# Kernel optimization log

Hardware: AMD Instinct MI355X
Metric: run time of the kernel (lower is better)

The kernel has to match this reference:

```python
import jax, jax.numpy as jnp
import numpy as np

N_NODES = 100000
D = 512
N_EDGES = 150000
N_PRED = 200000
EPS = 1e-12  # F.normalize default eps


def setup_inputs() -> dict:
    key = jax.random.key(0)
    ks = jax.random.split(key, 8)
    scale = 1.0 / np.sqrt(D)
    return {
        "x": jax.random.normal(ks[0], (N_NODES, D), dtype=jnp.float32),
        "edge_index": jax.random.randint(ks[1], (2, N_EDGES), 0, N_NODES, dtype=jnp.int64),
        "edge_weight": jax.random.uniform(ks[2], (N_EDGES,), dtype=jnp.float32),
        "pred_edges": jax.random.randint(ks[3], (2, N_PRED), 0, N_NODES, dtype=jnp.int64),
        "W1": jax.random.normal(ks[4], (D, D), dtype=jnp.float32) * scale,
        "b1": jnp.zeros((D,), jnp.float32),
        "W2": jax.random.normal(ks[5], (D, D), dtype=jnp.float32) * scale,
        "b2": jnp.zeros((D,), jnp.float32),
        "Wf": jax.random.normal(ks[6], (D, 2), dtype=jnp.float32) * scale,
        "bf": jnp.zeros((2,), jnp.float32),
    }


def gcn_conv(x, W, b, row, col, w, n):
    """PyG GCNConv with normalize=True: add self-loops (weight 1),
    symmetric deg^-1/2 normalization, message = norm * (xW)[row], scatter-add to col."""
    loop = jnp.arange(n)
    row2 = jnp.concatenate([row, loop])
    col2 = jnp.concatenate([col, loop])
    w2 = jnp.concatenate([w, jnp.ones((n,), x.dtype)])
    deg = jax.ops.segment_sum(w2, col2, num_segments=n)
    dinv = jnp.where(deg > 0, jax.lax.rsqrt(jnp.maximum(deg, EPS)), 0.0)
    norm = dinv[row2] * w2 * dinv[col2]  # [E+n]
    h = x @ W  # [n, out]
    out = jax.ops.segment_sum(norm[:, None] * h[row2], col2, num_segments=n)
    return out + b


def res_block(x, W, b, row, col, w, n):
    h = jax.nn.relu(gcn_conv(x, W, b, row, col, w, n))
    # dropout is identity in eval mode; then row-wise L2 normalize (F.normalize)
    nrm = jnp.maximum(jnp.linalg.norm(h, axis=1, keepdims=True), EPS)
    h = h / nrm
    return (h + x) * 0.5  # residual average (use_identity=True)


def reference(x, edge_index, edge_weight, pred_edges, W1, b1, W2, b2, Wf, bf):
    n = x.shape[0]
    row, col = edge_index[0], edge_index[1]
    h = res_block(x, W1, b1, row, col, edge_weight, n)
    h = res_block(h, W2, b2, row, col, edge_weight, n)
    h = gcn_conv(h, Wf, bf, row, col, edge_weight, n)
    h = jax.nn.log_softmax(h, axis=1)  # [n, 2]
    # DotProductPredictor, vectorized: h[u]*h[v]*(-1) per predictor edge
    return -(h[pred_edges[0]] * h[pred_edges[1]])  # [N_PRED, 2]
```

## Files before the change

kernel.cpp:

```cpp
#include <hip/hip_runtime.h>
#include <hip/hip_bf16.h>
#include <math.h>

typedef __bf16 bf16x8 __attribute__((ext_vector_type(8)));
typedef float f32x4 __attribute__((ext_vector_type(4)));
struct __align__(16) US8 { unsigned short v[8]; };

typedef __attribute__((address_space(1))) const unsigned short GUS;
typedef __attribute__((address_space(3))) unsigned short LUS;
static __device__ __forceinline__ void gload16(const unsigned short* g, unsigned short* l) {
    __builtin_amdgcn_global_load_lds((GUS*)g, (LUS*)l, 16, 0, 0);
}

static __device__ __forceinline__ unsigned short f2bf(float f) {
    unsigned int u = __float_as_uint(f);
    unsigned int r = (u + 0x7fffu + ((u >> 16) & 1u)) >> 16;
    return (unsigned short)r;
}
static __device__ __forceinline__ float bf2f(unsigned short u) {
    return __uint_as_float(((unsigned int)u) << 16);
}

__global__ void cvt_bf16_kernel(const float* __restrict__ in, unsigned short* __restrict__ outb,
                                int total8) {
    int i = blockIdx.x * 256 + threadIdx.x;
    if (i < total8) {
        const float4* p = (const float4*)(in + (size_t)i * 8);
        float4 a = p[0], b = p[1];
        US8 o;
        o.v[0] = f2bf(a.x); o.v[1] = f2bf(a.y); o.v[2] = f2bf(a.z); o.v[3] = f2bf(a.w);
        o.v[4] = f2bf(b.x); o.v[5] = f2bf(b.y); o.v[6] = f2bf(b.z); o.v[7] = f2bf(b.w);
        *(US8*)(outb + (size_t)i * 8) = o;
    }
}

__global__ void init_kernel(float* deg, int* cnt, int* cursor, int M) {
    int i = blockIdx.x * 256 + threadIdx.x;
    if (i < M) { deg[i] = 1.0f; cnt[i] = 0; cursor[i] = 0; }
}
__global__ void deg_cnt_kernel(const int* __restrict__ ei, const float* __restrict__ ew,
                               float* deg, int* cnt, int E) {
    int e = blockIdx.x * 256 + threadIdx.x;
    if (e < E) {
        int c = ei[E + e];
        atomicAdd(&deg[c], ew[e]);
        atomicAdd(&cnt[c], 1);
    }
}
__global__ void dinv_kernel(const float* __restrict__ deg, float* dinv, int M) {
    int i = blockIdx.x * 256 + threadIdx.x;
    if (i < M) dinv[i] = rsqrtf(deg[i]);
}

__global__ void chunk_sum_kernel(const int* __restrict__ cnt, int* partial, int M) {
    __shared__ int sd[256];
    int t = threadIdx.x;
    int i = blockIdx.x * 256 + t;
    sd[t] = (i < M) ? cnt[i] : 0;
    __syncthreads();
    for (int s = 128; s > 0; s >>= 1) {
        if (t < s) sd[t] += sd[t + s];
        __syncthreads();
    }
    if (t == 0) partial[blockIdx.x] = sd[0];
}
__global__ void scan_partial_kernel(int* partial, int NB) {
    __shared__ int sd[512];
    int t = threadIdx.x;
    int v = (t < NB) ? partial[t] : 0;
    sd[t] = v;
    __syncthreads();
    for (int o = 1; o < 512; o <<= 1) {
        int add = (t >= o) ? sd[t - o] : 0;
        __syncthreads();
        sd[t] += add;
        __syncthreads();
    }
    if (t < NB) partial[t] = sd[t] - v;
}
__global__ void rowptr_kernel(const int* __restrict__ cnt, const int* __restrict__ partial,
                              int* rowptr, int M, int E) {
    __shared__ int sd[256];
    int t = threadIdx.x;
    int i = blockIdx.x * 256 + t;
    int v = (i < M) ? cnt[i] : 0;
    sd[t] = v;
    __syncthreads();
    for (int o = 1; o < 256; o <<= 1) {
        int add = (t >= o) ? sd[t - o] : 0;
        __syncthreads();
        sd[t] += add;
        __syncthreads();
    }
    if (i < M) rowptr[i] = partial[blockIdx.x] + sd[t] - v;
    if (i == M - 1) rowptr[M] = E;
}
__global__ void csr_fill_kernel(const int* __restrict__ ei, const float* __restrict__ ew,
                                const float* __restrict__ dinv, const int* __restrict__ rowptr,
                                int* cursor, int* src, float* cf, int E) {
    int e = blockIdx.x * 256 + threadIdx.x;
    if (e < E) {
        int r = ei[e], c = ei[E + e];
        int k = atomicAdd(&cursor[c], 1);
        int pos = rowptr[c] + k;
        src[pos] = r;
        cf[pos] = dinv[r] * ew[e] * dinv[c];
    }
}

__global__ void agg_gather_kernel(const unsigned short* __restrict__ xin, const int* __restrict__ rowptr,
                                  const int* __restrict__ src, const float* __restrict__ cf,
                                  const float* __restrict__ dinv,
                                  unsigned short* __restrict__ abf, int M) {
    int row = blockIdx.x * 4 + (threadIdx.x >> 6);
    if (row >= M) return;
    int lane = threadIdx.x & 63;
    US8 v = *(const US8*)(xin + ((size_t)row << 9) + lane * 8);
    float d = dinv[row];
    float s = d * d;
    float a[8];
    #pragma unroll
    for (int t = 0; t < 8; t++) a[t] = s * bf2f(v.v[t]);
    int beg = rowptr[row], end = rowptr[row + 1];
    for (int j = beg; j < end; j++) {
        int r = src[j];
        float coef = cf[j];
        US8 u = *(const US8*)(xin + ((size_t)r << 9) + lane * 8);
        #pragma unroll
        for (int t = 0; t < 8; t++) a[t] += coef * bf2f(u.v[t]);
    }
    US8 o;
    #pragma unroll
    for (int t = 0; t < 8; t++) o.v[t] = f2bf(a[t]);
    *(US8*)(abf + ((size_t)row << 9) + lane * 8) = o;
}

__global__ void transpose_cvt_kernel(const float* __restrict__ W, unsigned short* __restrict__ BT) {
    int idx = blockIdx.x * 256 + threadIdx.x;
    int n = idx >> 9, k = idx & 511;
    BT[idx] = f2bf(W[k * 512 + n]);
}

__global__ __launch_bounds__(512, 4) void gemm_epi_kernel(
    const unsigned short* __restrict__ A,
    const unsigned short* __restrict__ BT,
    const float* __restrict__ bias,
    const unsigned short* __restrict__ xin,
    unsigned short* __restrict__ outp,
    int M) {
    __shared__ __align__(16) unsigned short As[2][64 * 32];
    __shared__ __align__(16) unsigned short Bs[2][512 * 32];
    __shared__ float red[8 * 64];
    __shared__ float invn[64];

    const int tid  = threadIdx.x;
    const int m0   = blockIdx.x * 64;
    const int wave = tid >> 6;
    const int lane = tid & 63;
    const int q    = lane >> 4;
    const int r    = lane & 15;

    f32x4 acc[4][4];
    #pragma unroll
    for (int mt = 0; mt < 4; mt++)
        #pragma unroll
        for (int nt = 0; nt < 4; nt++) acc[mt][nt] = (f32x4){0.f, 0.f, 0.f, 0.f};

    const int fr  = (r + (r >> 2)) & 3;
    const int kcp = q ^ fr;

    auto stage = [&](int ks, int buf) {
        const int k0 = ks * 32;
        unsigned short* Ab = &As[buf][0];
        unsigned short* Bb = &Bs[buf][0];
        #pragma unroll
        for (int j = 0; j < 4; j++) {
            int c0 = j * 512 + wave * 64;
            int c  = c0 + lane;
            if (c0 < 256) {
                int row = c >> 2, kl = c & 3;
                int kc = kl ^ ((row + (row >> 2)) & 3);
                gload16(A + (((size_t)(m0 + row)) << 9) + k0 + kc * 8, Ab + c0 * 8);
            } else {
                int cb = c - 256, cb0 = c0 - 256;
                int n = cb >> 2, kl = cb & 3;
                int kc = kl ^ ((n + (n >> 2)) & 3);
                gload16(BT + (((size_t)n) << 9) + k0 + kc * 8, Bb + cb0 * 8);
            }
        }
        if (wave < 4) {
            int cb0 = 1792 + wave * 64;
            int cb = cb0 + lane;
            int n = cb >> 2, kl = cb & 3;
            int kc = kl ^ ((n + (n >> 2)) & 3);
            gload16(BT + (((size_t)n) << 9) + k0 + kc * 8, Bb + cb0 * 8);
        }
    };

    stage(0, 0);
    for (int ks = 0; ks < 16; ks++) {
        const int cur = ks & 1;
        __syncthreads();
        if (ks < 15) stage(ks + 1, cur ^ 1);

        bf16x8 af[4];
        #pragma unroll
        for (int mt = 0; mt < 4; mt++)
            af[mt] = __builtin_bit_cast(bf16x8,
                *(const US8*)&As[cur][((mt * 16 + r) << 5) + kcp * 8]);
        #pragma unroll
        for (int nt = 0; nt < 4; nt++) {
            bf16x8 bfr = __builtin_bit_cast(bf16x8,
                *(const US8*)&Bs[cur][((wave * 64 + nt * 16 + r) << 5) + kcp * 8]);
            #pragma unroll
            for (int mt = 0; mt < 4; mt++)
                acc[mt][nt] = __builtin_amdgcn_mfma_f32_16x16x32_bf16(af[mt], bfr, acc[mt][nt], 0, 0, 0);
        }
    }

    float bs[4];
    #pragma unroll
    for (int nt = 0; nt < 4; nt++) bs[nt] = bias[wave * 64 + nt * 16 + r];

    float ss[4][4];
    #pragma unroll
    for (int mt = 0; mt < 4; mt++) {
        #pragma unroll
        for (int reg = 0; reg < 4; reg++) {
            float s = 0.f;
            #pragma unroll
            for (int nt = 0; nt < 4; nt++) {
                float t = fmaxf(acc[mt][nt][reg] + bs[nt], 0.f);
                acc[mt][nt][reg] = t;
                s += t * t;
            }
            ss[mt][reg] = s;
        }
    }
    #pragma unroll
    for (int mt = 0; mt < 4; mt++)
        #pragma unroll
        for (int reg = 0; reg < 4; reg++) {
            float s = ss[mt][reg];
            s += __shfl_xor(s, 1, 64);
            s += __shfl_xor(s, 2, 64);
            s += __shfl_xor(s, 4, 64);
            s += __shfl_xor(s, 8, 64);
            ss[mt][reg] = s;
        }
    if (r == 0) {
        #pragma unroll
        for (int mt = 0; mt < 4; mt++)
            #pragma unroll
            for (int reg = 0; reg < 4; reg++)
                red[wave * 64 + mt * 16 + q * 4 + reg] = ss[mt][reg];
    }
    __syncthreads();
    if (tid < 64) {
        float s = 0.f;
        #pragma unroll
        for (int w = 0; w < 8; w++) s += red[w * 64 + tid];
        invn[tid] = 1.0f / fmaxf(sqrtf(s), 1e-12f);
    }
    __syncthreads();

    #pragma unroll
    for (int mt = 0; mt < 4; mt++) {
        #pragma unroll
        for (int reg = 0; reg < 4; reg++) {
            int m = mt * 16 + q * 4 + reg;
            int gm = m0 + m;
            if (gm < M) {
                float inv = invn[m];
                #pragma unroll
                for (int nt = 0; nt < 4; nt++) {
                    int col = wave * 64 + nt * 16 + r;
                    size_t idx = ((size_t)gm << 9) + col;
                    outp[idx] = f2bf((acc[mt][nt][reg] * inv + bf2f(xin[idx])) * 0.5f);
                }
            }
        }
    }
}

__global__ void proj_kernel(const unsigned short* __restrict__ x3, const float* __restrict__ Wf,
                            float* __restrict__ p, int M) {
    __shared__ float w0[512], w1[512];
    int tid = threadIdx.x;
    for (int j = tid; j < 512; j += 256) { w0[j] = Wf[j * 2]; w1[j] = Wf[j * 2 + 1]; }
    __syncthreads();
    int row = blockIdx.x * 4 + (tid >> 6);
    if (row >= M) return;
    int lane = tid & 63;
    US8 v = *(const US8*)(x3 + ((size_t)row << 9) + lane * 8);
    int j0 = lane * 8;
    float s0 = 0.f, s1 = 0.f;
    #pragma unroll
    for (int t = 0; t < 8; t++) {
        float a = bf2f(v.v[t]);
        s0 += a * w0[j0 + t];
        s1 += a * w1[j0 + t];
    }
    #pragma unroll
    for (int off = 32; off > 0; off >>= 1) {
        s0 += __shfl_xor(s0, off, 64);
        s1 += __shfl_xor(s1, off, 64);
    }
    if (lane == 0) { p[row * 2] = s0; p[row * 2 + 1] = s1; }
}

__global__ void final_self_kernel(const float* __restrict__ p, const float* __restrict__ dinv,
                                  float* pa, int M) {
    int i = blockIdx.x * 256 + threadIdx.x;
    if (i < M) {
        float d = dinv[i]; float s = d * d;
        pa[i * 2] = s * p[i * 2];
        pa[i * 2 + 1] = s * p[i * 2 + 1];
    }
}
__global__ void final_edge_kernel(const float* __restrict__ p, const int* __restrict__ ei,
                                  const float* __restrict__ ew, const float* __restrict__ dinv,
                                  float* pa, int E) {
    int e = blockIdx.x * 256 + threadIdx.x;
    if (e < E) {
        int r = ei[e], c = ei[E + e];
        float coef = dinv[r] * ew[e] * dinv[c];
        atomicAdd(&pa[c * 2], coef * p[r * 2]);
        atomicAdd(&pa[c * 2 + 1], coef * p[r * 2 + 1]);
    }
}
__global__ void lsm_kernel(const float* __restrict__ pa, const float* __restrict__ bfv,
                           float* __restrict__ logp, int M) {
    int i = blockIdx.x * 256 + threadIdx.x;
    if (i < M) {
        float a = pa[i * 2] + bfv[0], b = pa[i * 2 + 1] + bfv[1];
        float m = fmaxf(a, b);
        float lse = m + logf(expf(a - m) + expf(b - m));
        logp[i * 2] = a - lse;
        logp[i * 2 + 1] = b - lse;
    }
}
__global__ void pred_kernel(const float* __restrict__ logp, const int* __restrict__ pe,
                            float* __restrict__ out, int P) {
    int i = blockIdx.x * 256 + threadIdx.x;
    if (i < P) {
        int u = pe[i], v = pe[P + i];
        out[i * 2]     = -(logp[u * 2] * logp[v * 2]);
        out[i * 2 + 1] = -(logp[u * 2 + 1] * logp[v * 2 + 1]);
    }
}

extern "C" void kernel_launch(void* const* d_in, const int* in_sizes, int n_in,
                              void* d_out, int out_size, void* d_ws, size_t ws_size,
                              hipStream_t stream) {
    const float* x   = (const float*)d_in[0];
    const int*   ei  = (const int*)d_in[1];
    const float* ew  = (const float*)d_in[2];
    const int*   pe  = (const int*)d_in[3];
    const float* W1  = (const float*)d_in[4];
    const float* b1  = (const float*)d_in[5];
    const float* W2  = (const float*)d_in[6];
    const float* b2  = (const float*)d_in[7];
    const float* Wf  = (const float*)d_in[8];
    const float* bfv = (const float*)d_in[9];
    float* out = (float*)d_out;

    const int M = in_sizes[0] / 512;
    const int E = in_sizes[2];
    const int P = in_sizes[3] / 2;
    const int NB = (M + 255) / 256;
    const int MB64 = (M + 63) / 64;
    const int Mpad = MB64 * 64;

    char* ws = (char*)d_ws;
    size_t off = 0;
    auto alloc = [&](size_t bytes) { void* q = ws + off; off += (bytes + 255) & ~(size_t)255; return q; };
    float* deg    = (float*)alloc((size_t)M * 4);
    float* dinv   = (float*)alloc((size_t)M * 4);
    int*   cnt    = (int*)alloc((size_t)M * 4);
    int*   cursor = (int*)alloc((size_t)M * 4);
    int*   rowptr = (int*)alloc((size_t)(M + 1) * 4);
    int*   partial= (int*)alloc((size_t)NB * 4);
    int*   srcidx = (int*)alloc((size_t)E * 4);
    float* cf     = (float*)alloc((size_t)E * 4);
    unsigned short* xb  = (unsigned short*)alloc((size_t)M * 512 * 2);
    unsigned short* x2b = (unsigned short*)alloc((size_t)M * 512 * 2);
    unsigned short* x3b = (unsigned short*)alloc((size_t)M * 512 * 2);
    unsigned short* abf = (unsigned short*)alloc((size_t)Mpad * 512 * 2);
    unsigned short* BT1 = (unsigned short*)alloc(512 * 512 * 2);
    unsigned short* BT2 = (unsigned short*)alloc(512 * 512 * 2);
    float* p    = (float*)alloc((size_t)M * 2 * 4);
    float* pa   = (float*)alloc((size_t)M * 2 * 4);
    float* logp = (float*)alloc((size_t)M * 2 * 4);

    const int nthr = 256;

    cvt_bf16_kernel<<<(M * 64 + 255) / 256, nthr, 0, stream>>>(x, xb, M * 64);
    init_kernel<<<NB, nthr, 0, stream>>>(deg, cnt, cursor, M);
    deg_cnt_kernel<<<(E + 255) / 256, nthr, 0, stream>>>(ei, ew, deg, cnt, E);
    dinv_kernel<<<NB, nthr, 0, stream>>>(deg, dinv, M);
    chunk_sum_kernel<<<NB, nthr, 0, stream>>>(cnt, partial, M);
    scan_partial_kernel<<<1, 512, 0, stream>>>(partial, NB);
    rowptr_kernel<<<NB, nthr, 0, stream>>>(cnt, partial, rowptr, M, E);
    csr_fill_kernel<<<(E + 255) / 256, nthr, 0, stream>>>(ei, ew, dinv, rowptr, cursor, srcidx, cf, E);
    transpose_cvt_kernel<<<1024, nthr, 0, stream>>>(W1, BT1);
    transpose_cvt_kernel<<<1024, nthr, 0, stream>>>(W2, BT2);

    agg_gather_kernel<<<(M + 3) / 4, nthr, 0, stream>>>(xb, rowptr, srcidx, cf, dinv, abf, M);
    gemm_epi_kernel<<<MB64, 512, 0, stream>>>(abf, BT1, b1, xb, x2b, M);

    agg_gather_kernel<<<(M + 3) / 4, nthr, 0, stream>>>(x2b, rowptr, srcidx, cf, dinv, abf, M);
    gemm_epi_kernel<<<MB64, 512, 0, stream>>>(abf, BT2, b2, x2b, x3b, M);

    proj_kernel<<<(M + 3) / 4, nthr, 0, stream>>>(x3b, Wf, p, M);
    final_self_kernel<<<NB, nthr, 0, stream>>>(p, dinv, pa, M);
    final_edge_kernel<<<(E + 255) / 256, nthr, 0, stream>>>(p, ei, ew, dinv, pa, E);
    lsm_kernel<<<NB, nthr, 0, stream>>>(pa, bfv, logp, M);
    pred_kernel<<<(P + 255) / 256, nthr, 0, stream>>>(logp, pe, out, P);
}
```

Baseline: 801.1 us.

## Fuse sparse gather aggregation into GEMM kernel via full A tile in LDS

Replaces the separate aggregation kernel and GEMM with one kernel per layer. Each block gathers neighbor rows for its 64 output rows directly into a swizzled 64x512 bf16 LDS tile, then runs the MFMA GEMM and normalize/residual epilogue. This removes the round trip of the aggregated matrix through global memory and one launch per layer, and adds one-ahead software prefetching in the neighbor loop. In exchange, LDS use grows to about 64KB A plus 64KB B per block, which lowers occupancy. The gather phase also runs with only 8 waves per block before the GEMM can start.

```diff
diff --git a/kernel.cpp b/kernel.cpp
--- a/kernel.cpp
+++ b/kernel.cpp
@@ -108,47 +108,23 @@
     }
 }
 
-__global__ void agg_gather_kernel(const unsigned short* __restrict__ xin, const int* __restrict__ rowptr,
-                                  const int* __restrict__ src, const float* __restrict__ cf,
-                                  const float* __restrict__ dinv,
-                                  unsigned short* __restrict__ abf, int M) {
-    int row = blockIdx.x * 4 + (threadIdx.x >> 6);
-    if (row >= M) return;
-    int lane = threadIdx.x & 63;
-    US8 v = *(const US8*)(xin + ((size_t)row << 9) + lane * 8);
-    float d = dinv[row];
-    float s = d * d;
-    float a[8];
-    #pragma unroll
-    for (int t = 0; t < 8; t++) a[t] = s * bf2f(v.v[t]);
-    int beg = rowptr[row], end = rowptr[row + 1];
-    for (int j = beg; j < end; j++) {
-        int r = src[j];
-        float coef = cf[j];
-        US8 u = *(const US8*)(xin + ((size_t)r << 9) + lane * 8);
-        #pragma unroll
-        for (int t = 0; t < 8; t++) a[t] += coef * bf2f(u.v[t]);
-    }
-    US8 o;
-    #pragma unroll
-    for (int t = 0; t < 8; t++) o.v[t] = f2bf(a[t]);
-    *(US8*)(abf + ((size_t)row << 9) + lane * 8) = o;
-}
-
 __global__ void transpose_cvt_kernel(const float* __restrict__ W, unsigned short* __restrict__ BT) {
     int idx = blockIdx.x * 256 + threadIdx.x;
     int n = idx >> 9, k = idx & 511;
     BT[idx] = f2bf(W[k * 512 + n]);
 }
 
-__global__ __launch_bounds__(512, 4) void gemm_epi_kernel(
-    const unsigned short* __restrict__ A,
+__global__ __launch_bounds__(512) void fused_layer_kernel(
+    const unsigned short* __restrict__ xb,
+    const int* __restrict__ rowptr,
+    const int* __restrict__ src,
+    const float* __restrict__ cf,
+    const float* __restrict__ dinv,
     const unsigned short* __restrict__ BT,
     const float* __restrict__ bias,
-    const unsigned short* __restrict__ xin,
     unsigned short* __restrict__ outp,
     int M) {
-    __shared__ __align__(16) unsigned short As[2][64 * 32];
+    __shared__ __align__(16) unsigned short As[64 * 512];
     __shared__ __align__(16) unsigned short Bs[2][512 * 32];
     __shared__ float red[8 * 64];
     __shared__ float invn[64];
@@ -160,58 +136,81 @@
     const int q    = lane >> 4;
     const int r    = lane & 15;
 
-    f32x4 acc[4][4];
-    #pragma unroll
-    for (int mt = 0; mt < 4; mt++)
-        #pragma unroll
-        for (int nt = 0; nt < 4; nt++) acc[mt][nt] = (f32x4){0.f, 0.f, 0.f, 0.f};
-
-    const int fr  = (r + (r >> 2)) & 3;
-    const int kcp = q ^ fr;
-
-    auto stage = [&](int ks, int buf) {
+    auto stageB = [&](int ks, int buf) {
         const int k0 = ks * 32;
-        unsigned short* Ab = &As[buf][0];
         unsigned short* Bb = &Bs[buf][0];
         #pragma unroll
         for (int j = 0; j < 4; j++) {
             int c0 = j * 512 + wave * 64;
             int c  = c0 + lane;
-            if (c0 < 256) {
-                int row = c >> 2, kl = c & 3;
-                int kc = kl ^ ((row + (row >> 2)) & 3);
-                gload16(A + (((size_t)(m0 + row)) << 9) + k0 + kc * 8, Ab + c0 * 8);
-            } else {
-                int cb = c - 256, cb0 = c0 - 256;
-                int n = cb >> 2, kl = cb & 3;
-                int kc = kl ^ ((n + (n >> 2)) & 3);
-                gload16(BT + (((size_t)n) << 9) + k0 + kc * 8, Bb + cb0 * 8);
+            int n = c >> 2, kl = c & 3;
+            int kc = kl ^ ((n + (n >> 2)) & 3);
+            gload16(BT + (((size_t)n) << 9) + k0 + kc * 8, Bb + c0 * 8);
+        }
+    };
+
+    stageB(0, 0);
+    stageB(1, 1);
+
+    for (int i = 0; i < 8; i++) {
+        int m = wave * 8 + i;
+        int gm = m0 + m;
+        float a[8];
+        if (gm < M) {
+            float d = dinv[gm];
+            float s = d * d;
+            US8 v = *(const US8*)(xb + ((size_t)gm << 9) + lane * 8);
+            #pragma unroll
+            for (int t = 0; t < 8; t++) a[t] = s * bf2f(v.v[t]);
+            int j = rowptr[gm], jend = rowptr[gm + 1];
+            if (j < jend) {
+                US8 u = *(const US8*)(xb + ((size_t)src[j] << 9) + lane * 8);
+                float cv = cf[j];
+                while (j < jend) {
+                    int jn = j + 1;
+                    US8 un; float cn = 0.f;
+                    if (jn < jend) {
+                        cn = cf[jn];
+                        un = *(const US8*)(xb + ((size_t)src[jn] << 9) + lane * 8);
+                    }
+                    #pragma unroll
+                    for (int t = 0; t < 8; t++) a[t] += cv * bf2f(u.v[t]);
+                    u = un; cv = cn; j = jn;
+                }
             }
-        }
-        if (wave < 4) {
-            int cb0 = 1792 + wave * 64;
-            int cb = cb0 + lane;
-            int n = cb >> 2, kl = cb & 3;
-            int kc = kl ^ ((n + (n >> 2)) & 3);
-            gload16(BT + (((size_t)n) << 9) + k0 + kc * 8, Bb + cb0 * 8);
-        }
-    };
-
-    stage(0, 0);
+        } else {
+            #pragma unroll
+            for (int t = 0; t < 8; t++) a[t] = 0.f;
+        }
+        US8 o;
+        #pragma unroll
+        for (int t = 0; t < 8; t++) o.v[t] = f2bf(a[t]);
+        *(US8*)&As[(m << 9) + ((lane ^ (m & 7)) << 3)] = o;
+    }
+
+    f32x4 acc[4][4];
+    #pragma unroll
+    for (int mt = 0; mt < 4; mt++)
+        #pragma unroll
+        for (int nt = 0; nt < 4; nt++) acc[mt][nt] = (f32x4){0.f, 0.f, 0.f, 0.f};
+
+    const int frB = (r + (r >> 2)) & 3;
+    const int frA = r & 7;
+
     for (int ks = 0; ks < 16; ks++) {
+        __syncthreads();
+        if (ks >= 1 && ks + 1 < 16) stageB(ks + 1, (ks + 1) & 1);
+
         const int cur = ks & 1;
-        __syncthreads();
-        if (ks < 15) stage(ks + 1, cur ^ 1);
-
         bf16x8 af[4];
         #pragma unroll
         for (int mt = 0; mt < 4; mt++)
             af[mt] = __builtin_bit_cast(bf16x8,
-                *(const US8*)&As[cur][((mt * 16 + r) << 5) + kcp * 8]);
+                *(const US8*)&As[((mt * 16 + r) << 9) + (((ks * 4 + q) ^ frA) << 3)]);
         #pragma unroll
         for (int nt = 0; nt < 4; nt++) {
             bf16x8 bfr = __builtin_bit_cast(bf16x8,
-                *(const US8*)&Bs[cur][((wave * 64 + nt * 16 + r) << 5) + kcp * 8]);
+                *(const US8*)&Bs[cur][((wave * 64 + nt * 16 + r) << 5) + ((q ^ frB) << 3)]);
             #pragma unroll
             for (int mt = 0; mt < 4; mt++)
                 acc[mt][nt] = __builtin_amdgcn_mfma_f32_16x16x32_bf16(af[mt], bfr, acc[mt][nt], 0, 0, 0);
@@ -276,7 +275,7 @@
                 for (int nt = 0; nt < 4; nt++) {
                     int col = wave * 64 + nt * 16 + r;
                     size_t idx = ((size_t)gm << 9) + col;
-                    outp[idx] = f2bf((acc[mt][nt][reg] * inv + bf2f(xin[idx])) * 0.5f);
+                    outp[idx] = f2bf((acc[mt][nt][reg] * inv + bf2f(xb[idx])) * 0.5f);
                 }
             }
         }
@@ -370,7 +369,6 @@
     const int P = in_sizes[3] / 2;
     const int NB = (M + 255) / 256;
     const int MB64 = (M + 63) / 64;
-    const int Mpad = MB64 * 64;
 
     char* ws = (char*)d_ws;
     size_t off = 0;
@@ -386,7 +384,6 @@
     unsigned short* xb  = (unsigned short*)alloc((size_t)M * 512 * 2);
     unsigned short* x2b = (unsigned short*)alloc((size_t)M * 512 * 2);
     unsigned short* x3b = (unsigned short*)alloc((size_t)M * 512 * 2);
-    unsigned short* abf = (unsigned short*)alloc((size_t)Mpad * 512 * 2);
     unsigned short* BT1 = (unsigned short*)alloc(512 * 512 * 2);
     unsigned short* BT2 = (unsigned short*)alloc(512 * 512 * 2);
     float* p    = (float*)alloc((size_t)M * 2 * 4);
@@ -406,11 +403,9 @@
     transpose_cvt_kernel<<<1024, nthr, 0, stream>>>(W1, BT1);
     transpose_cvt_kernel<<<1024, nthr, 0, stream>>>(W2, BT2);
 
-    agg_gather_kernel<<<(M + 3) / 4, nthr, 0, stream>>>(xb, rowptr, srcidx, cf, dinv, abf, M);
-    gemm_epi_kernel<<<MB64, 512, 0, stream>>>(abf, BT1, b1, xb, x2b, M);
-
-    agg_gather_kernel<<<(M + 3) / 4, nthr, 0, stream>>>(x2b, rowptr, srcidx, cf, dinv, abf, M);
-    gemm_epi_kernel<<<MB64, 512, 0, stream>>>(abf, BT2, b2, x2b, x3b, M);
+    fused_layer_kernel<<<MB64, 512, 0, stream>>>(xb, rowptr, srcidx, cf, dinv, BT1, b1, x2b, M);
+
+    fused_layer_kernel<<<MB64, 512, 0, stream>>>(x2b, rowptr, srcidx, cf, dinv, BT2, b2, x3b, M);
 
     proj_kernel<<<(M + 3) / 4, nthr, 0, stream>>>(x3b, Wf, p, M);
     final_self_kernel<<<NB, nthr, 0, stream>>>(p, dinv, pa, M);
```

Result: slower. 846.2 us (+5.6%).
